# Kernel tuning notes

Hardware: AMD Instinct MI355X
Metric: run time of the kernel (lower is better)

## Reference

```python
import jax, jax.numpy as jnp
import numpy as np

T, S, B, D, H, DH, DI = 1024, 1024, 4, 1024, 16, 64, 4096
SCALE = 1.0 / (DH ** 0.5)


def _ln(x, g, b, eps=1e-5):
    m = jnp.mean(x, axis=-1, keepdims=True)
    v = jnp.mean((x - m) ** 2, axis=-1, keepdims=True)
    return (x - m) * jax.lax.rsqrt(v + eps) * g + b


def setup_inputs() -> dict:
    key = jax.random.key(0)
    ks = jax.random.split(key, 16)
    s = 0.02
    inp = {
        "dec_inp": jax.random.normal(ks[0], (T, B, D), jnp.float32),
        "enc_out": jax.random.normal(ks[1], (T, B, D), jnp.float32),
        # causal mask for self-attn: [qlen, klen, bsz], True = masked
        "dec_mask": jnp.broadcast_to(jnp.triu(jnp.ones((T, T), bool), 1)[:, :, None], (T, T, B)),
        # encoder padding mask: [klen, bsz], last 128 positions padded
        "enc_mask": jnp.broadcast_to((jnp.arange(S) >= S - 128)[:, None], (S, B)),
        # self-attn params
        "W_q1": jax.random.normal(ks[2], (D, H * DH), jnp.float32) * s,
        "W_kv1": jax.random.normal(ks[3], (D, 2 * H * DH), jnp.float32) * s,
        "W_o1": jax.random.normal(ks[4], (H * DH, D), jnp.float32) * s,
        "g1": jnp.ones((D,), jnp.float32), "b1": jnp.zeros((D,), jnp.float32),
        # cross-attn params
        "W_q2": jax.random.normal(ks[5], (D, H * DH), jnp.float32) * s,
        "W_kv2": jax.random.normal(ks[6], (D, 2 * H * DH), jnp.float32) * s,
        "W_o2": jax.random.normal(ks[7], (H * DH, D), jnp.float32) * s,
        "g2": jnp.ones((D,), jnp.float32), "b2": jnp.zeros((D,), jnp.float32),
        # FFN params
        "W_ff1": jax.random.normal(ks[8], (D, DI), jnp.float32) * s,
        "b_ff1": jnp.zeros((DI,), jnp.float32),
        "W_ff2": jax.random.normal(ks[9], (DI, D), jnp.float32) * s,
        "b_ff2": jnp.zeros((D,), jnp.float32),
        "g3": jnp.ones((D,), jnp.float32), "b3": jnp.zeros((D,), jnp.float32),
    }
    return inp


def reference(dec_inp, enc_out, dec_mask, enc_mask,
              W_q1, W_kv1, W_o1, g1, b1,
              W_q2, W_kv2, W_o2, g2, b2,
              W_ff1, b_ff1, W_ff2, b_ff2, g3, b3):
    # ---- self-attention (MultiHeadAttn, pre_lnorm=True, mems=None) ----
    # NOTE: q is computed from the UN-normalized h; k,v from LN(c) — faithful to source.
    c = _ln(dec_inp, g1, b1)
    q = (dec_inp @ W_q1).reshape(T, B, H, DH)
    kv = (c @ W_kv1)
    k, v = jnp.split(kv, 2, axis=-1)
    k = k.reshape(T, B, H, DH)
    v = v.reshape(T, B, H, DH)
    score = jnp.einsum('ibnd,jbnd->ijbn', q, k) * SCALE  # [T,T,B,H]
    score = jnp.where(dec_mask[:, :, :, None], -jnp.inf, score)
    prob = jax.nn.softmax(score, axis=1)
    vec = jnp.einsum('ijbn,jbnd->ibnd', prob, v).reshape(T, B, H * DH)
    out1 = dec_inp + vec @ W_o1

    # ---- cross-attention (ContextMultiHeadAttn, pre_lnorm=True) ----
    # NOTE: residual uses the layer-normed h (source reassigns h = layer_norm(h)).
    h2 = _ln(out1, g2, b2)
    q2 = (h2 @ W_q2).reshape(T, B, H, DH)
    kv2 = enc_out @ W_kv2  # enc_out is NOT layer-normed in source
    k2, v2 = jnp.split(kv2, 2, axis=-1)
    k2 = k2.reshape(S, B, H, DH)
    v2 = v2.reshape(S, B, H, DH)
    score2 = jnp.einsum('ibnd,jbnd->ijbn', q2, k2) * SCALE  # [T,S,B,H]
    score2 = jnp.where(enc_mask[None, :, :, None], -10000.0, score2)
    prob2 = jax.nn.softmax(score2, axis=1)
    vec2 = jnp.einsum('ijbn,jbnd->ibnd', prob2, v2).reshape(T, B, H * DH)
    out2 = h2 + vec2 @ W_o2

    # ---- position-wise FFN (pre_lnorm) ----
    h3 = _ln(out2, g3, b3)
    core = jax.nn.gelu(h3 @ W_ff1 + b_ff1, approximate=False) @ W_ff2 + b_ff2
    return out2 + core
```

## Files before the change

### kernel.cpp

```cpp
#include <hip/hip_runtime.h>
#include <hip/hip_bf16.h>

#define T_ 1024
#define S_ 1024
#define B_ 4
#define D_ 1024
#define H_ 16
#define DH_ 64
#define DI_ 4096
#define NTOK 4096

typedef __attribute__((ext_vector_type(8))) short bf16x8;
typedef __attribute__((ext_vector_type(4))) float f32x4;

__device__ __forceinline__ short f2bf(float f) {
  unsigned u = __builtin_bit_cast(unsigned, f);
  u += 0x7fffu + ((u >> 16) & 1u);
  return (short)(u >> 16);
}

__device__ __forceinline__ void g2l16(const void* g, void* l) {
  __builtin_amdgcn_global_load_lds(
      (const __attribute__((address_space(1))) unsigned int*)g,
      (__attribute__((address_space(3))) unsigned int*)l, 16, 0, 0);
}

template <int EPI, int BN>
__global__ __launch_bounds__(256, 2) void gemm_bt(
    const short* __restrict__ A, const short* __restrict__ Bt,
    float* __restrict__ outF, short* __restrict__ outB,
    const float* __restrict__ res, const float* __restrict__ bias,
    short* __restrict__ Kgp, short* __restrict__ Vgp,
    int M, int N, int K) {
  constexpr int WCOLS = BN / 64;
  constexpr int MI = (WCOLS == 2) ? 4 : 2;
  constexpr int BLOADS = BN / 32;
  __shared__ short sA[2][128 * 64];
  __shared__ short sB[2][BN * 64];
  const int tid = threadIdx.x;
  const int lane = tid & 63;
  const int w = tid >> 6;
  const int wr = (WCOLS == 2) ? (w >> 1) : w;
  const int wc = (WCOLS == 2) ? (w & 1) : 0;
  const int r15 = lane & 15, g4 = lane >> 4;
  const size_t row0 = (size_t)blockIdx.x * 128;
  const size_t col0 = (size_t)blockIdx.y * BN;

  f32x4 acc[MI][4];
#pragma unroll
  for (int i = 0; i < MI; i++)
#pragma unroll
    for (int j = 0; j < 4; j++) acc[i][j] = (f32x4){0.f, 0.f, 0.f, 0.f};

  auto stage = [&](int buf, int kt) {
    const int k0 = kt << 6;
#pragma unroll
    for (int i = 0; i < 4; i++) {
      int flat = i * 256 + tid;
      int row = flat >> 3;
      int col = k0 + (((flat & 7) ^ (row & 7)) << 3);
      g2l16(A + (row0 + row) * (size_t)K + col, &sA[buf][(i * 256 + w * 64) * 8]);
    }
#pragma unroll
    for (int i = 0; i < BLOADS; i++) {
      int flat = i * 256 + tid;
      int row = flat >> 3;
      int col = k0 + (((flat & 7) ^ (row & 7)) << 3);
      g2l16(Bt + (col0 + row) * (size_t)K + col, &sB[buf][(i * 256 + w * 64) * 8]);
    }
  };

  stage(0, 0);
  __syncthreads();

  const int nk = K >> 6;
  for (int kt = 0; kt < nk; ++kt) {
    const int cur = kt & 1;
    if (kt + 1 < nk) stage(cur ^ 1, kt + 1);
#pragma unroll
    for (int kk = 0; kk < 2; ++kk) {
      bf16x8 af[MI], bfr[4];
#pragma unroll
      for (int mi = 0; mi < MI; mi++) {
        int rowA = wr * (MI * 16) + mi * 16 + r15;
        af[mi] = *(const bf16x8*)(&sA[cur][rowA * 64 +
                                           (((kk * 4 + g4) ^ (rowA & 7)) << 3)]);
      }
#pragma unroll
      for (int ni = 0; ni < 4; ni++) {
        int rowB = wc * 64 + ni * 16 + r15;
        bfr[ni] = *(const bf16x8*)(&sB[cur][rowB * 64 +
                                            (((kk * 4 + g4) ^ (rowB & 7)) << 3)]);
      }
#pragma unroll
      for (int mi = 0; mi < MI; mi++)
#pragma unroll
        for (int ni = 0; ni < 4; ni++)
          acc[mi][ni] = __builtin_amdgcn_mfma_f32_16x16x32_bf16(af[mi], bfr[ni],
                                                                acc[mi][ni], 0, 0, 0);
    }
    __syncthreads();
  }

#pragma unroll
  for (int mi = 0; mi < MI; mi++) {
    size_t row = row0 + wr * (MI * 16) + mi * 16 + (g4 << 2);
#pragma unroll
    for (int ni = 0; ni < 4; ni++) {
      size_t col = col0 + wc * 64 + ni * 16 + r15;
      float bcol = (EPI == 2 || EPI == 3) ? bias[col] : 0.f;
#pragma unroll
      for (int r = 0; r < 4; r++) {
        size_t idx = (row + r) * (size_t)N + col;
        float v = acc[mi][ni][r];
        if (EPI == 0) {
          outB[idx] = f2bf(v);
        } else if (EPI == 1) {
          outF[idx] = v + res[idx];
        } else if (EPI == 2) {
          float x = v + bcol;
          float gl = 0.5f * x * (1.f + erff(x * 0.70710678118654752f));
          outB[idx] = f2bf(gl);
        } else if (EPI == 3) {
          outF[idx] = v + bcol + res[idx];
        } else {
          int tt = (int)(row + r) >> 2;
          int bb = (int)(row + r) & 3;
          int cc = (int)col;
          if (cc < 1024) {
            int hh = cc >> 6, dd = cc & 63;
            size_t base = (size_t)(bb * 16 + hh) * 65536 + (size_t)tt * 64;
            Kgp[base + ((((dd >> 3) ^ (tt & 7)) << 3) | (dd & 7))] = f2bf(v * 0.125f);
          } else {
            int hh = (cc >> 6) - 16, dd = cc & 63;
            size_t base = (size_t)(bb * 16 + hh) * 65536 + (size_t)(tt >> 6) * 4096;
            Vgp[base + ((tt >> 3) & 7) * 512 + dd * 8 + (tt & 7)] = f2bf(v);
          }
        }
      }
    }
  }
}

template <int MODE>
__global__ __launch_bounds__(256, 2) void attn_k2(const short* __restrict__ Qm,
                                                  const short* __restrict__ Kg,
                                                  const short* __restrict__ Vg,
                                                  short* __restrict__ Om) {
  __shared__ short Kl[2][4096];
  __shared__ short Vl[2][4096];
  __shared__ short Pl[4][2048];
  const int tid = threadIdx.x;
  const int lane = tid & 63;
  const int w = tid >> 6;
  const int r15 = lane & 15, g4 = lane >> 4;
  const int bh = blockIdx.x;
  const int qt = blockIdx.y;
  const int b = bh >> 4, h = bh & 15;
  const int qbase = qt * 128 + w * 32;
  const int ktDiag = qbase >> 6;

  bf16x8 qf[2][2];
#pragma unroll
  for (int g = 0; g < 2; g++)
#pragma unroll
    for (int hf = 0; hf < 2; hf++) {
      int row = qbase + g * 16 + r15;
      qf[g][hf] = *(const bf16x8*)(Qm + ((size_t)(row * 4 + b)) * 1024 + h * 64 +
                                   hf * 32 + g4 * 8);
    }

  const size_t kvbase = (size_t)bh * 65536;
  const int nkt = (MODE == 0) ? (2 * qt + 2) : 14;

  f32x4 o[2][4];
#pragma unroll
  for (int g = 0; g < 2; g++)
#pragma unroll
    for (int ni = 0; ni < 4; ni++) o[g][ni] = (f32x4){0.f, 0.f, 0.f, 0.f};
  float mrun[2][4], lrun[2][4];
#pragma unroll
  for (int g = 0; g < 2; g++)
#pragma unroll
    for (int r = 0; r < 4; r++) { mrun[g][r] = -1e30f; lrun[g][r] = 0.f; }

  {
    const size_t tb = kvbase;
#pragma unroll
    for (int i = 0; i < 2; i++) {
      g2l16(Kg + tb + (size_t)(i * 256 + tid) * 8, &Kl[0][(i * 256 + w * 64) * 8]);
      g2l16(Vg + tb + (size_t)(i * 256 + tid) * 8, &Vl[0][(i * 256 + w * 64) * 8]);
    }
  }
  __syncthreads();

  for (int kt = 0; kt < nkt; kt++) {
    const int cur = kt & 1;
    if (kt + 1 < nkt) {
      const size_t tb = kvbase + (size_t)(kt + 1) * 4096;
#pragma unroll
      for (int i = 0; i < 2; i++) {
        g2l16(Kg + tb + (size_t)(i * 256 + tid) * 8,
              &Kl[cur ^ 1][(i * 256 + w * 64) * 8]);
        g2l16(Vg + tb + (size_t)(i * 256 + tid) * 8,
              &Vl[cur ^ 1][(i * 256 + w * 64) * 8]);
      }
    }

    const bool active = (MODE == 1) || (kt * 64 <= qbase + 31);
    if (active) {
      bf16x8 kb[4][2];
#pragma unroll
      for (int ni = 0; ni < 4; ni++) {
        int row = ni * 16 + r15;
        kb[ni][0] = *(const bf16x8*)(&Kl[cur][row * 64 + ((g4 ^ (row & 7)) << 3)]);
        kb[ni][1] =
            *(const bf16x8*)(&Kl[cur][row * 64 + (((g4 + 4) ^ (row & 7)) << 3)]);
      }
      f32x4 sf[2][4];
#pragma unroll
      for (int g = 0; g < 2; g++)
#pragma unroll
        for (int ni = 0; ni < 4; ni++) {
          f32x4 s = (f32x4){0.f, 0.f, 0.f, 0.f};
          s = __builtin_amdgcn_mfma_f32_16x16x32_bf16(qf[g][0], kb[ni][0], s, 0, 0, 0);
          s = __builtin_amdgcn_mfma_f32_16x16x32_bf16(qf[g][1], kb[ni][1], s, 0, 0, 0);
          sf[g][ni] = s;
        }
      if (MODE == 0 && kt >= ktDiag) {
#pragma unroll
        for (int g = 0; g < 2; g++)
#pragma unroll
          for (int ni = 0; ni < 4; ni++)
#pragma unroll
            for (int r = 0; r < 4; r++) {
              int q = qbase + g * 16 + g4 * 4 + r;
              int key = kt * 64 + ni * 16 + r15;
              if (key > q) sf[g][ni][r] = -1e30f;
            }
      }
#pragma unroll
      for (int g = 0; g < 2; g++) {
        float corr[4];
#pragma unroll
        for (int r = 0; r < 4; r++) {
          float m = fmaxf(fmaxf(sf[g][0][r], sf[g][1][r]),
                          fmaxf(sf[g][2][r], sf[g][3][r]));
          m = fmaxf(m, __shfl_xor(m, 1));
          m = fmaxf(m, __shfl_xor(m, 2));
          m = fmaxf(m, __shfl_xor(m, 4));
          m = fmaxf(m, __shfl_xor(m, 8));
          float mn = fmaxf(mrun[g][r], m);
          corr[r] = __expf(mrun[g][r] - mn);
          mrun[g][r] = mn;
        }
        float rs[4] = {0.f, 0.f, 0.f, 0.f};
#pragma unroll
        for (int ni = 0; ni < 4; ni++)
#pragma unroll
          for (int r = 0; r < 4; r++) {
            float p = __expf(sf[g][ni][r] - mrun[g][r]);
            sf[g][ni][r] = p;
            rs[r] += p;
          }
#pragma unroll
        for (int r = 0; r < 4; r++) {
          rs[r] += __shfl_xor(rs[r], 1);
          rs[r] += __shfl_xor(rs[r], 2);
          rs[r] += __shfl_xor(rs[r], 4);
          rs[r] += __shfl_xor(rs[r], 8);
          lrun[g][r] = lrun[g][r] * corr[r] + rs[r];
        }
#pragma unroll
        for (int ni = 0; ni < 4; ni++)
#pragma unroll
          for (int r = 0; r < 4; r++) o[g][ni][r] *= corr[r];
#pragma unroll
        for (int ni = 0; ni < 4; ni++)
#pragma unroll
          for (int r = 0; r < 4; r++) {
            int qr = g * 16 + g4 * 4 + r;
            int key = ni * 16 + r15;
            Pl[w][qr * 64 + ((((key >> 3) ^ ((qr >> 1) & 7)) << 3) | (key & 7))] =
                f2bf(sf[g][ni][r]);
          }
      }
#pragma unroll
      for (int kk = 0; kk < 2; kk++) {
        int gw = kk * 4 + g4;
        bf16x8 pa0 = *(const bf16x8*)(&Pl[w][r15 * 64 + ((gw ^ ((r15 >> 1) & 7)) << 3)]);
        bf16x8 pa1 =
            *(const bf16x8*)(&Pl[w][(16 + r15) * 64 + ((gw ^ ((r15 >> 1) & 7)) << 3)]);
#pragma unroll
        for (int ni = 0; ni < 4; ni++) {
          bf16x8 vb = *(const bf16x8*)(&Vl[cur][(gw * 64 + ni * 16 + r15) * 8]);
          o[0][ni] = __builtin_amdgcn_mfma_f32_16x16x32_bf16(pa0, vb, o[0][ni], 0, 0, 0);
          o[1][ni] = __builtin_amdgcn_mfma_f32_16x16x32_bf16(pa1, vb, o[1][ni], 0, 0, 0);
        }
      }
    }
    __syncthreads();
  }

#pragma unroll
  for (int g = 0; g < 2; g++) {
    float inv[4];
#pragma unroll
    for (int r = 0; r < 4; r++) inv[r] = 1.f / lrun[g][r];
#pragma unroll
    for (int ni = 0; ni < 4; ni++) {
      int col = h * 64 + ni * 16 + r15;
#pragma unroll
      for (int r = 0; r < 4; r++) {
        int tg = qbase + g * 16 + g4 * 4 + r;
        Om[((size_t)(tg * 4 + b)) * 1024 + col] = f2bf(o[g][ni][r] * inv[r]);
      }
    }
  }
}

__global__ __launch_bounds__(256) void ln_k(const float* __restrict__ x,
                                            const float* __restrict__ gw,
                                            const float* __restrict__ bw,
                                            float* __restrict__ outF,
                                            short* __restrict__ outB,
                                            short* __restrict__ outXB) {
  const int row = blockIdx.x, tid = threadIdx.x;
  const float4 v = ((const float4*)(x + (size_t)row * 1024))[tid];
  float s = v.x + v.y + v.z + v.w;
  float ss = v.x * v.x + v.y * v.y + v.z * v.z + v.w * v.w;
#pragma unroll
  for (int d = 32; d >= 1; d >>= 1) {
    s += __shfl_xor(s, d);
    ss += __shfl_xor(ss, d);
  }
  __shared__ float red[8];
  const int w = tid >> 6;
  if ((tid & 63) == 0) { red[w] = s; red[4 + w] = ss; }
  __syncthreads();
  s = red[0] + red[1] + red[2] + red[3];
  ss = red[4] + red[5] + red[6] + red[7];
  const float mean = s * (1.f / 1024.f);
  const float var = ss * (1.f / 1024.f) - mean * mean;
  const float rstd = rsqrtf(var + 1e-5f);
  const float4 gv = ((const float4*)gw)[tid];
  const float4 bv = ((const float4*)bw)[tid];
  float4 y;
  y.x = (v.x - mean) * rstd * gv.x + bv.x;
  y.y = (v.y - mean) * rstd * gv.y + bv.y;
  y.z = (v.z - mean) * rstd * gv.z + bv.z;
  y.w = (v.w - mean) * rstd * gv.w + bv.w;
  if (outF) ((float4*)(outF + (size_t)row * 1024))[tid] = y;
  if (outB) {
    short4 ob;
    ob.x = f2bf(y.x); ob.y = f2bf(y.y); ob.z = f2bf(y.z); ob.w = f2bf(y.w);
    ((short4*)(outB + (size_t)row * 1024))[tid] = ob;
  }
  if (outXB) {
    short4 ob;
    ob.x = f2bf(v.x); ob.y = f2bf(v.y); ob.z = f2bf(v.z); ob.w = f2bf(v.w);
    ((short4*)(outXB + (size_t)row * 1024))[tid] = ob;
  }
}

__global__ __launch_bounds__(256) void cvt_bf16(const float* __restrict__ in,
                                                short* __restrict__ out) {
  const size_t i = (size_t)blockIdx.x * 256 + threadIdx.x;
  const float4 v = ((const float4*)in)[i];
  short4 ob;
  ob.x = f2bf(v.x); ob.y = f2bf(v.y); ob.z = f2bf(v.z); ob.w = f2bf(v.w);
  ((short4*)out)[i] = ob;
}

__global__ __launch_bounds__(256) void tr_cvt(const float* __restrict__ in,
                                              short* __restrict__ out, int K, int N) {
  __shared__ float t[64][65];
  const int tid = threadIdx.x;
  const int k0 = blockIdx.x * 64, n0 = blockIdx.y * 64;
#pragma unroll
  for (int i = 0; i < 16; i++) {
    int flat = i * 256 + tid;
    int r = flat >> 6, c = flat & 63;
    t[r][c] = in[(size_t)(k0 + r) * N + n0 + c];
  }
  __syncthreads();
#pragma unroll
  for (int i = 0; i < 16; i++) {
    int flat = i * 256 + tid;
    int r = flat >> 6, c = flat & 63;
    out[(size_t)(n0 + r) * K + k0 + c] = f2bf(t[c][r]);
  }
}

extern "C" void kernel_launch(void* const* d_in, const int* in_sizes, int n_in,
                              void* d_out, int out_size, void* d_ws, size_t ws_size,
                              hipStream_t stream) {
  const float* dec_inp = (const float*)d_in[0];
  const float* enc_out = (const float*)d_in[1];
  const float* W_q1 = (const float*)d_in[4];
  const float* W_kv1 = (const float*)d_in[5];
  const float* W_o1 = (const float*)d_in[6];
  const float* g1 = (const float*)d_in[7];
  const float* b1 = (const float*)d_in[8];
  const float* W_q2 = (const float*)d_in[9];
  const float* W_kv2 = (const float*)d_in[10];
  const float* W_o2 = (const float*)d_in[11];
  const float* g2 = (const float*)d_in[12];
  const float* b2 = (const float*)d_in[13];
  const float* W_ff1 = (const float*)d_in[14];
  const float* b_ff1 = (const float*)d_in[15];
  const float* W_ff2 = (const float*)d_in[16];
  const float* b_ff2 = (const float*)d_in[17];
  const float* g3 = (const float*)d_in[18];
  const float* b3 = (const float*)d_in[19];
  float* out = (float*)d_out;

  char* ws = (char*)d_ws;
  size_t off = 0;
  auto alloc = [&](size_t bytes) -> void* {
    void* p = ws + off;
    off += (bytes + 255) & ~(size_t)255;
    return p;
  };
  short* Wq1t = (short*)alloc(1024ull * 1024 * 2);
  short* Wkv1t = (short*)alloc(2048ull * 1024 * 2);
  short* Wo1t = (short*)alloc(1024ull * 1024 * 2);
  short* Wq2t = (short*)alloc(1024ull * 1024 * 2);
  short* Wkv2t = (short*)alloc(2048ull * 1024 * 2);
  short* Wo2t = (short*)alloc(1024ull * 1024 * 2);
  short* Wff1t = (short*)alloc(4096ull * 1024 * 2);
  short* Wff2t = (short*)alloc(1024ull * 4096 * 2);
  short* Xbf = (short*)alloc((size_t)NTOK * 1024 * 2);
  short* Ebf = (short*)alloc((size_t)NTOK * 1024 * 2);
  short* Cbf = (short*)alloc((size_t)NTOK * 1024 * 2);
  short* Qb = (short*)alloc((size_t)NTOK * 1024 * 2);
  short* Kg = (short*)alloc(64ull * 65536 * 2);
  short* Vg = (short*)alloc(64ull * 65536 * 2);
  short* VECb = (short*)alloc((size_t)NTOK * 1024 * 2);
  float* OUT1 = (float*)alloc((size_t)NTOK * 1024 * 4);
  float* H2f = (float*)alloc((size_t)NTOK * 1024 * 4);
  float* OUT2 = (float*)alloc((size_t)NTOK * 1024 * 4);
  short* FF1 = (short*)alloc((size_t)NTOK * 4096 * 2);
  short* H2b = Xbf;
  short* H3b = Cbf;

  dim3 blk(256, 1, 1);

  tr_cvt<<<dim3(16, 16), blk, 0, stream>>>(W_q1, Wq1t, 1024, 1024);
  tr_cvt<<<dim3(16, 32), blk, 0, stream>>>(W_kv1, Wkv1t, 1024, 2048);
  tr_cvt<<<dim3(16, 16), blk, 0, stream>>>(W_o1, Wo1t, 1024, 1024);
  tr_cvt<<<dim3(16, 16), blk, 0, stream>>>(W_q2, Wq2t, 1024, 1024);
  tr_cvt<<<dim3(16, 32), blk, 0, stream>>>(W_kv2, Wkv2t, 1024, 2048);
  tr_cvt<<<dim3(16, 16), blk, 0, stream>>>(W_o2, Wo2t, 1024, 1024);
  tr_cvt<<<dim3(16, 64), blk, 0, stream>>>(W_ff1, Wff1t, 1024, 4096);
  tr_cvt<<<dim3(64, 16), blk, 0, stream>>>(W_ff2, Wff2t, 4096, 1024);

  cvt_bf16<<<4096, blk, 0, stream>>>(enc_out, Ebf);
  ln_k<<<4096, blk, 0, stream>>>(dec_inp, g1, b1, nullptr, Cbf, Xbf);

  gemm_bt<0, 64><<<dim3(32, 16), blk, 0, stream>>>(
      Xbf, Wq1t, nullptr, Qb, nullptr, nullptr, nullptr, nullptr, 4096, 1024, 1024);
  gemm_bt<4, 128><<<dim3(32, 16), blk, 0, stream>>>(
      Cbf, Wkv1t, nullptr, nullptr, nullptr, nullptr, Kg, Vg, 4096, 2048, 1024);
  attn_k2<0><<<dim3(64, 8), blk, 0, stream>>>(Qb, Kg, Vg, VECb);
  gemm_bt<1, 64><<<dim3(32, 16), blk, 0, stream>>>(
      VECb, Wo1t, OUT1, nullptr, dec_inp, nullptr, nullptr, nullptr, 4096, 1024, 1024);
  ln_k<<<4096, blk, 0, stream>>>(OUT1, g2, b2, H2f, H2b, nullptr);
  gemm_bt<0, 64><<<dim3(32, 16), blk, 0, stream>>>(
      H2b, Wq2t, nullptr, Qb, nullptr, nullptr, nullptr, nullptr, 4096, 1024, 1024);
  gemm_bt<4, 128><<<dim3(32, 16), blk, 0, stream>>>(
      Ebf, Wkv2t, nullptr, nullptr, nullptr, nullptr, Kg, Vg, 4096, 2048, 1024);
  attn_k2<1><<<dim3(64, 8), blk, 0, stream>>>(Qb, Kg, Vg, VECb);
  gemm_bt<1, 64><<<dim3(32, 16), blk, 0, stream>>>(
      VECb, Wo2t, OUT2, nullptr, H2f, nullptr, nullptr, nullptr, 4096, 1024, 1024);
  ln_k<<<4096, blk, 0, stream>>>(OUT2, g3, b3, nullptr, H3b, nullptr);
  gemm_bt<2, 128><<<dim3(32, 32), blk, 0, stream>>>(
      H3b, Wff1t, nullptr, FF1, nullptr, b_ff1, nullptr, nullptr, 4096, 4096, 1024);
  gemm_bt<3, 64><<<dim3(32, 16), blk, 0, stream>>>(
      FF1, Wff2t, out, nullptr, OUT2, b_ff2, nullptr, nullptr, 4096, 1024, 4096);
}
```

Baseline: 375.8 us.

## Add 256x256-tile 8-wave pipelined GEMM kernel for FFN1

Adds a new GEMM kernel with 256x256 output tiles and 512 threads (8 waves). It splits each K-step into four quadrant phases that interleave LDS fragment reads, async global-to-LDS prefetch of half-tiles, and MFMA bursts raised with s_setprio. It replaces the 128x128 GEMM used for the FF1 projection with GELU epilogue, aiming for more operand reuse per tile and better overlap of loads with compute. In exchange it uses more LDS and registers, and only 256 blocks are launched, which may leave the GPU underfilled.

```diff
diff --git a/kernel.cpp b/kernel.cpp
--- a/kernel.cpp
+++ b/kernel.cpp
@@ -23,6 +23,201 @@
   __builtin_amdgcn_global_load_lds(
       (const __attribute__((address_space(1))) unsigned int*)g,
       (__attribute__((address_space(3))) unsigned int*)l, 16, 0, 0);
+}
+
+__device__ __forceinline__ void bar() {
+  asm volatile("" ::: "memory");
+  __builtin_amdgcn_s_barrier();
+  asm volatile("" ::: "memory");
+}
+
+template <int EPI>
+__global__ __launch_bounds__(512, 2) void gemm8p(
+    const short* __restrict__ A, const short* __restrict__ Bt,
+    float* __restrict__ outF, short* __restrict__ outB,
+    const float* __restrict__ res, const float* __restrict__ bias,
+    int M, int N, int K) {
+  __shared__ short sA[2][256 * 64];
+  __shared__ short sB[2][256 * 64];
+  const int tid = threadIdx.x;
+  const int lane = tid & 63;
+  const int w = tid >> 6;
+  const int wm = w >> 2, wn = w & 3;
+  const int r15 = lane & 15, g4 = lane >> 4;
+  const size_t row0 = (size_t)blockIdx.x * 256;
+  const size_t col0 = (size_t)blockIdx.y * 256;
+
+  f32x4 acc[8][4];
+#pragma unroll
+  for (int i = 0; i < 8; i++)
+#pragma unroll
+    for (int j = 0; j < 4; j++) acc[i][j] = (f32x4){0.f, 0.f, 0.f, 0.f};
+
+  auto stageA = [&](int buf, int s, int kt) {
+    const int k0 = kt << 6;
+#pragma unroll
+    for (int j = 0; j < 2; ++j) {
+      const int c = j * 8 + w;
+      const int rb = ((c >> 3) << 7) + (s << 6) + ((c & 7) << 3);
+      const int row = rb + (lane >> 3);
+      const int col = k0 + (((lane & 7) ^ (row & 7)) << 3);
+      g2l16(A + (row0 + row) * (size_t)K + col, &sA[buf][rb * 64]);
+    }
+  };
+  auto stageB = [&](int buf, int s, int kt) {
+    const int k0 = kt << 6;
+#pragma unroll
+    for (int j = 0; j < 2; ++j) {
+      const int c = j * 8 + w;
+      const int rb = ((c >> 2) << 6) + (s << 5) + ((c & 3) << 3);
+      const int row = rb + (lane >> 3);
+      const int col = k0 + (((lane & 7) ^ (row & 7)) << 3);
+      g2l16(Bt + (col0 + row) * (size_t)K + col, &sB[buf][rb * 64]);
+    }
+  };
+
+  const int nk = K >> 6;
+  stageA(0, 0, 0); stageA(0, 1, 0); stageB(0, 0, 0); stageB(0, 1, 0);
+  if (nk > 1) {
+    stageA(1, 0, 1); stageB(1, 1, 1);
+    asm volatile("s_waitcnt vmcnt(4)" ::: "memory");
+  } else {
+    asm volatile("s_waitcnt vmcnt(0)" ::: "memory");
+  }
+  bar();
+
+  bf16x8 af[4][2], bv[2][2];
+  for (int t = 0; t < nk; ++t) {
+    const int cur = t & 1;
+    const short* cA = sA[cur];
+    const short* cB = sB[cur];
+#pragma unroll
+    for (int mi = 0; mi < 4; mi++) {
+      const int rowA = wm * 128 + mi * 16 + r15;
+#pragma unroll
+      for (int kk = 0; kk < 2; kk++)
+        af[mi][kk] = *(const bf16x8*)(cA + rowA * 64 +
+                                      (((kk * 4 + g4) ^ (rowA & 7)) << 3));
+    }
+#pragma unroll
+    for (int ni = 0; ni < 2; ni++) {
+      const int rowB = wn * 64 + ni * 16 + r15;
+#pragma unroll
+      for (int kk = 0; kk < 2; kk++)
+        bv[ni][kk] = *(const bf16x8*)(cB + rowB * 64 +
+                                      (((kk * 4 + g4) ^ (rowB & 7)) << 3));
+    }
+    if (t + 1 < nk) stageA(cur ^ 1, 1, t + 1);
+    bar();
+    asm volatile("s_waitcnt lgkmcnt(0)" ::: "memory");
+    __builtin_amdgcn_s_setprio(1);
+#pragma unroll
+    for (int kk = 0; kk < 2; kk++)
+#pragma unroll
+      for (int mi = 0; mi < 4; mi++)
+#pragma unroll
+        for (int ni = 0; ni < 2; ni++)
+          acc[mi][ni] = __builtin_amdgcn_mfma_f32_16x16x32_bf16(
+              af[mi][kk], bv[ni][kk], acc[mi][ni], 0, 0, 0);
+    __builtin_amdgcn_s_setprio(0);
+    bar();
+#pragma unroll
+    for (int ni = 0; ni < 2; ni++) {
+      const int rowB = wn * 64 + (2 + ni) * 16 + r15;
+#pragma unroll
+      for (int kk = 0; kk < 2; kk++)
+        bv[ni][kk] = *(const bf16x8*)(cB + rowB * 64 +
+                                      (((kk * 4 + g4) ^ (rowB & 7)) << 3));
+    }
+    if (t + 1 < nk) stageB(cur ^ 1, 0, t + 1);
+    bar();
+    asm volatile("s_waitcnt lgkmcnt(0)" ::: "memory");
+    __builtin_amdgcn_s_setprio(1);
+#pragma unroll
+    for (int kk = 0; kk < 2; kk++)
+#pragma unroll
+      for (int mi = 0; mi < 4; mi++)
+#pragma unroll
+        for (int ni = 0; ni < 2; ni++)
+          acc[mi][2 + ni] = __builtin_amdgcn_mfma_f32_16x16x32_bf16(
+              af[mi][kk], bv[ni][kk], acc[mi][2 + ni], 0, 0, 0);
+    __builtin_amdgcn_s_setprio(0);
+    bar();
+#pragma unroll
+    for (int mi = 0; mi < 4; mi++) {
+      const int rowA = wm * 128 + (4 + mi) * 16 + r15;
+#pragma unroll
+      for (int kk = 0; kk < 2; kk++)
+        af[mi][kk] = *(const bf16x8*)(cA + rowA * 64 +
+                                      (((kk * 4 + g4) ^ (rowA & 7)) << 3));
+    }
+    if (t + 2 < nk) stageA(cur, 0, t + 2);
+    bar();
+    asm volatile("s_waitcnt lgkmcnt(0)" ::: "memory");
+    __builtin_amdgcn_s_setprio(1);
+#pragma unroll
+    for (int kk = 0; kk < 2; kk++)
+#pragma unroll
+      for (int mi = 0; mi < 4; mi++)
+#pragma unroll
+        for (int ni = 0; ni < 2; ni++)
+          acc[4 + mi][2 + ni] = __builtin_amdgcn_mfma_f32_16x16x32_bf16(
+              af[mi][kk], bv[ni][kk], acc[4 + mi][2 + ni], 0, 0, 0);
+    __builtin_amdgcn_s_setprio(0);
+    bar();
+#pragma unroll
+    for (int ni = 0; ni < 2; ni++) {
+      const int rowB = wn * 64 + ni * 16 + r15;
+#pragma unroll
+      for (int kk = 0; kk < 2; kk++)
+        bv[ni][kk] = *(const bf16x8*)(cB + rowB * 64 +
+                                      (((kk * 4 + g4) ^ (rowB & 7)) << 3));
+    }
+    if (t + 2 < nk) stageB(cur, 1, t + 2);
+    bar();
+    asm volatile("s_waitcnt lgkmcnt(0)" ::: "memory");
+    __builtin_amdgcn_s_setprio(1);
+#pragma unroll
+    for (int kk = 0; kk < 2; kk++)
+#pragma unroll
+      for (int mi = 0; mi < 4; mi++)
+#pragma unroll
+        for (int ni = 0; ni < 2; ni++)
+          acc[4 + mi][ni] = __builtin_amdgcn_mfma_f32_16x16x32_bf16(
+              af[mi][kk], bv[ni][kk], acc[4 + mi][ni], 0, 0, 0);
+    __builtin_amdgcn_s_setprio(0);
+    if (t + 2 < nk)
+      asm volatile("s_waitcnt vmcnt(4)" ::: "memory");
+    else if (t + 1 < nk)
+      asm volatile("s_waitcnt vmcnt(0)" ::: "memory");
+    bar();
+  }
+
+#pragma unroll
+  for (int mi = 0; mi < 8; mi++) {
+    size_t row = row0 + wm * 128 + mi * 16 + (g4 << 2);
+#pragma unroll
+    for (int ni = 0; ni < 4; ni++) {
+      size_t col = col0 + wn * 64 + ni * 16 + r15;
+      float bcol = (EPI == 2 || EPI == 3) ? bias[col] : 0.f;
+#pragma unroll
+      for (int r = 0; r < 4; r++) {
+        size_t idx = (row + r) * (size_t)N + col;
+        float v = acc[mi][ni][r];
+        if (EPI == 0) {
+          outB[idx] = f2bf(v);
+        } else if (EPI == 1) {
+          outF[idx] = v + res[idx];
+        } else if (EPI == 2) {
+          float x = v + bcol;
+          float gl = 0.5f * x * (1.f + erff(x * 0.70710678118654752f));
+          outB[idx] = f2bf(gl);
+        } else {
+          outF[idx] = v + bcol + res[idx];
+        }
+      }
+    }
+  }
 }
 
 template <int EPI, int BN>
@@ -474,8 +669,8 @@
   gemm_bt<1, 64><<<dim3(32, 16), blk, 0, stream>>>(
       VECb, Wo2t, OUT2, nullptr, H2f, nullptr, nullptr, nullptr, 4096, 1024, 1024);
   ln_k<<<4096, blk, 0, stream>>>(OUT2, g3, b3, nullptr, H3b, nullptr);
-  gemm_bt<2, 128><<<dim3(32, 32), blk, 0, stream>>>(
-      H3b, Wff1t, nullptr, FF1, nullptr, b_ff1, nullptr, nullptr, 4096, 4096, 1024);
+  gemm8p<2><<<dim3(16, 16), dim3(512, 1, 1), 0, stream>>>(
+      H3b, Wff1t, nullptr, FF1, nullptr, b_ff1, 4096, 4096, 1024);
   gemm_bt<3, 64><<<dim3(32, 16), blk, 0, stream>>>(
       FF1, Wff2t, out, nullptr, OUT2, b_ff2, nullptr, nullptr, 4096, 1024, 4096);
 }
```

Measured after the change: 382.5 us. No clear change (+1.8%).
